# Optimization experiments

Measured on AMD Instinct MI355X. Metric: run time of the kernel, lower is better.

## Reference

```python
import jax, jax.numpy as jnp
import numpy as np

NUM_HEADS = 8

def _heads(x, B, N, H):
    # [B, N, C] -> [B, H, N, d]
    return x.reshape(B, N, H, -1).transpose(0, 2, 1, 3)

def setup_inputs() -> dict:
    key = jax.random.key(0)
    k1, k2, k3, k4 = jax.random.split(key, 4)
    B, N, C = 8, 4096, 512
    x1 = jax.random.normal(k1, (B, N, C), dtype=jnp.float32)
    x2 = jax.random.normal(k2, (B, N, C), dtype=jnp.float32)
    # nn.Linear weights stored as [in, out] for x @ W
    Wkv1 = jax.random.normal(k3, (C, 2 * C), dtype=jnp.float32) * (C ** -0.5)
    Wkv2 = jax.random.normal(k4, (C, 2 * C), dtype=jnp.float32) * (C ** -0.5)
    return {"x1": x1, "x2": x2, "Wkv1": Wkv1, "Wkv2": Wkv2}

def reference(x1, x2, Wkv1, Wkv2):
    B, N, C = x1.shape
    H = NUM_HEADS
    d = C // H
    scale = d ** -0.5

    q1 = _heads(x1, B, N, H)                      # [B,H,N,d]
    q2 = _heads(x2, B, N, H)

    kv1 = (x1 @ Wkv1).reshape(B, N, 2, H, d).transpose(2, 0, 3, 1, 4)
    kv2 = (x2 @ Wkv2).reshape(B, N, 2, H, d).transpose(2, 0, 3, 1, 4)
    k1, v1 = kv1[0], kv1[1]                       # [B,H,N,d]
    k2, v2 = kv2[0], kv2[1]

    # contexts: K^T V over tokens -> small [B,H,d,d]
    ctx1 = jnp.einsum('bhnd,bhne->bhde', k1, v1) * scale
    ctx2 = jnp.einsum('bhnd,bhne->bhde', k2, v2) * scale

    # softmax over dim=-2 (the first d axis), then Q @ ctx
    a1 = jnp.einsum('bhnd,bhde->bhne', q1, jax.nn.softmax(ctx2, axis=-2))
    a2 = jnp.einsum('bhnd,bhde->bhne', q2, jax.nn.softmax(ctx1, axis=-2))

    out1 = a1.transpose(0, 2, 1, 3).reshape(B, N, C)
    out2 = a2.transpose(0, 2, 1, 3).reshape(B, N, C)
    return out1, out2
```

## Files before the change

kernel.cpp:

```cpp
#include <hip/hip_runtime.h>
#include <hip/hip_bf16.h>

typedef __bf16   bf16x8 __attribute__((ext_vector_type(8)));
typedef _Float16 f16x8  __attribute__((ext_vector_type(8)));
typedef _Float16 f16x4  __attribute__((ext_vector_type(4)));
typedef float    f32x4  __attribute__((ext_vector_type(4)));

#define NTOK 4096
#define CDIM 512
#define HEADS 8
#define HD 64

__device__ __forceinline__ void gload_lds16(const void* g, void* l) {
    __builtin_amdgcn_global_load_lds((const __attribute__((address_space(1))) void*)g,
                                     (__attribute__((address_space(3))) void*)l, 16, 0, 0);
}

__global__ __launch_bounds__(256, 3) void xpose_kernel(const float* __restrict__ x1,
                                                       const float* __restrict__ x2,
                                                       const float* __restrict__ Wkv1,
                                                       const float* __restrict__ Wkv2,
                                                       _Float16* __restrict__ xt,
                                                       _Float16* __restrict__ wvt) {
    const int t = threadIdx.x, w = t >> 6, l = t & 63;

    if (blockIdx.x >= 64) {
        if (blockIdx.z >= 8) return;
        const int s = blockIdx.x - 64;
        const float* W = (s ? Wkv2 : Wkv1);
        const int k0 = blockIdx.z * 64;
        const int j = blockIdx.y * 256 + w * 64 + l;

        f16x8 vh[8];
        #pragma unroll
        for (int q = 0; q < 64; ++q) {
            float v = W[(size_t)(k0 + q) * (2 * CDIM) + CDIM + j];
            vh[q >> 3][q & 7] = (_Float16)v;
        }
        _Float16* dh = wvt + ((size_t)s * CDIM + j) * CDIM + k0;
        #pragma unroll
        for (int q = 0; q < 8; ++q)
            *(f16x8*)&dh[q * 8] = vh[q];
        return;
    }

    const int kb = blockIdx.x, cb = blockIdx.y, sb = blockIdx.z;
    const int s = sb >> 3, b = sb & 7;
    const float* xs = (s ? x2 : x1) + (size_t)b * NTOK * CDIM
                    + (size_t)kb * 64 * CDIM + cb * 256;

    __shared__ _Float16 lds[64 * 256];

    float4 v[16];
    #pragma unroll
    for (int i = 0; i < 16; ++i) {
        const int n = 4 * i + w;
        v[i] = *(const float4*)&xs[(size_t)n * CDIM + l * 4];
    }
    #pragma unroll
    for (int i = 0; i < 16; ++i) {
        const int n = 4 * i + w;
        f16x4 p = {(_Float16)v[i].x, (_Float16)v[i].y, (_Float16)v[i].z, (_Float16)v[i].w};
        *(f16x4*)&lds[n * 256 + ((l ^ (n >> 3)) << 2)] = p;
    }
    __syncthreads();

    const int kk8 = (l & 7);
    _Float16* dst = xt + ((size_t)(sb * 64 + kb) * CDIM + cb * 256) * 64;
    #pragma unroll
    for (int q = 0; q < 8; ++q) {
        const int cw = 64 * w + 8 * q + (l >> 3);
        const int c4s = (cw >> 2) ^ kk8, c2 = cw & 3;
        const int base = (c4s << 2) + c2 + kk8 * 8 * 256;
        f16x8 o;
        #pragma unroll
        for (int j = 0; j < 8; ++j)
            o[j] = lds[base + j * 256];
        *(f16x8*)&dst[(size_t)cw * 64 + kk8 * 8] = o;
    }
}

__global__ __launch_bounds__(256) void gram_kernel(const _Float16* __restrict__ xt,
                                                   _Float16* __restrict__ GPh) {
    const int id = blockIdx.x;
    const int vid = (id & 7) * 64 + (id >> 3);
    const int sb = vid >> 5, rest = vid & 31;
    const int split = rest >> 4, tile = rest & 15;
    const int I0 = (tile >> 2) * 128, J0 = (tile & 3) * 128;
    const _Float16* xb = xt + (size_t)sb * CDIM * NTOK;

    __shared__ _Float16 Ih[2][128 * 64];
    __shared__ _Float16 Jh[2][128 * 64];

    const int t = threadIdx.x, w = t >> 6, l = t & 63;
    const int wm = w >> 1, wn = w & 1, l15 = l & 15, lk = l >> 4;
    const int colr = w * 8 + (l >> 3), pos = l & 7;

    f32x4 acc[4][4];
    #pragma unroll
    for (int f = 0; f < 4; ++f)
        #pragma unroll
        for (int g = 0; g < 4; ++g) acc[f][g] = (f32x4)(0.0f);

    auto STAGE = [&](int bufi, int it) {
        const _Float16* kb = xb + (size_t)(split * 32 + it) * CDIM * 64;
        #pragma unroll
        for (int r = 0; r < 4; ++r) {
            const int colw = r * 32 + colr;
            const int swz = ((pos ^ (colw & 7)) << 3);
            gload_lds16(kb + (size_t)(I0 + colw) * 64 + swz, &Ih[bufi][r * 2048 + w * 512]);
            gload_lds16(kb + (size_t)(J0 + colw) * 64 + swz, &Jh[bufi][r * 2048 + w * 512]);
        }
    };

    STAGE(0, 0);
    for (int it = 0; it < 32; ++it) {
        const int cur = it & 1;
        if (it < 31) {
            STAGE(cur ^ 1, it + 1);
            asm volatile("s_waitcnt vmcnt(8)" ::: "memory");
        } else {
            asm volatile("s_waitcnt vmcnt(0)" ::: "memory");
        }
        __builtin_amdgcn_s_barrier();

        const _Float16* Ib = &Ih[cur][0];
        const _Float16* Jb = &Jh[cur][0];
        __builtin_amdgcn_s_setprio(1);
        #pragma unroll
        for (int ks = 0; ks < 2; ++ks) {
            f16x8 a[4], bb[4];
            #pragma unroll
            for (int f = 0; f < 4; ++f) {
                const int i = wm * 64 + f * 16 + l15;
                a[f] = *(const f16x8*)&Ib[i * 64 + ((ks * 4 + lk) ^ (i & 7)) * 8];
            }
            #pragma unroll
            for (int g = 0; g < 4; ++g) {
                const int j = wn * 64 + g * 16 + l15;
                bb[g] = *(const f16x8*)&Jb[j * 64 + ((ks * 4 + lk) ^ (j & 7)) * 8];
            }
            #pragma unroll
            for (int f = 0; f < 4; ++f)
                #pragma unroll
                for (int g = 0; g < 4; ++g)
                    acc[f][g] = __builtin_amdgcn_mfma_f32_16x16x32_f16(a[f], bb[g], acc[f][g], 0, 0, 0);
        }
        __builtin_amdgcn_s_setprio(0);
        __builtin_amdgcn_s_barrier();
    }

    _Float16* Gout = GPh + ((size_t)split * 16 + sb) * CDIM * CDIM;
    #pragma unroll
    for (int f = 0; f < 4; ++f)
        #pragma unroll
        for (int g = 0; g < 4; ++g) {
            const int row0 = I0 + wm * 64 + f * 16 + lk * 4;
            const int col  = J0 + wn * 64 + g * 16 + l15;
            #pragma unroll
            for (int r = 0; r < 4; ++r)
                Gout[(size_t)(row0 + r) * CDIM + col] = (_Float16)acc[f][g][r];
        }
}

__global__ __launch_bounds__(256) void t_kernel(const _Float16* __restrict__ GPh,
                                                const _Float16* __restrict__ wvt,
                                                _Float16* __restrict__ TP) {
    const int id = blockIdx.x;
    const int vid = (id & 7) * 64 + (id >> 3);
    const int sb = vid >> 5, rest = vid & 31;
    const int ks2 = rest >> 4, tile = rest & 15;
    const int s = sb >> 3;
    const int I0 = (tile >> 2) * 128, J0 = (tile & 3) * 128;
    const _Float16* G0 = GPh + (size_t)sb * CDIM * CDIM;
    const _Float16* G1 = GPh + ((size_t)16 + sb) * CDIM * CDIM;
    const _Float16* Bv = wvt + (size_t)s * CDIM * CDIM;

    __shared__ _Float16 Ah[128 * 64];
    __shared__ _Float16 Jh[128 * 64];

    const int t = threadIdx.x, w = t >> 6, l = t & 63;
    const int wm = w >> 1, wn = w & 1, l15 = l & 15, lk = l >> 4;
    const int colr = w * 8 + (l >> 3), pos = l & 7;

    f32x4 acc[4][4];
    #pragma unroll
    for (int f = 0; f < 4; ++f)
        #pragma unroll
        for (int g = 0; g < 4; ++g) acc[f][g] = (f32x4)(0.0f);

    for (int it = 0; it < 4; ++it) {
        const int k0 = ks2 * 256 + it * 64;
        __syncthreads();
        #pragma unroll
        for (int r = 0; r < 4; ++r) {
            const int col = r * 32 + colr;
            const int swz = ((pos ^ (col & 7)) << 3);
            gload_lds16(Bv + (size_t)(J0 + col) * CDIM + k0 + swz, &Jh[r * 2048 + w * 512]);
        }
        #pragma unroll
        for (int r = 0; r < 4; ++r) {
            const int i = r * 32 + (t >> 3), ch = t & 7;
            f16x8 a0 = *(const f16x8*)&G0[(size_t)(I0 + i) * CDIM + k0 + ch * 8];
            f16x8 a1 = *(const f16x8*)&G1[(size_t)(I0 + i) * CDIM + k0 + ch * 8];
            f16x8 sum = a0 + a1;
            *(f16x8*)&Ah[i * 64 + ((ch ^ (i & 7)) << 3)] = sum;
        }
        __syncthreads();
        __builtin_amdgcn_s_setprio(1);
        #pragma unroll
        for (int ks = 0; ks < 2; ++ks) {
            f16x8 a[4], bb[4];
            #pragma unroll
            for (int f = 0; f < 4; ++f) {
                const int i = wm * 64 + f * 16 + l15;
                a[f] = *(const f16x8*)&Ah[i * 64 + ((ks * 4 + lk) ^ (i & 7)) * 8];
            }
            #pragma unroll
            for (int g = 0; g < 4; ++g) {
                const int j = wn * 64 + g * 16 + l15;
                bb[g] = *(const f16x8*)&Jh[j * 64 + ((ks * 4 + lk) ^ (j & 7)) * 8];
            }
            #pragma unroll
            for (int f = 0; f < 4; ++f)
                #pragma unroll
                for (int g = 0; g < 4; ++g)
                    acc[f][g] = __builtin_amdgcn_mfma_f32_16x16x32_f16(a[f], bb[g], acc[f][g], 0, 0, 0);
        }
        __builtin_amdgcn_s_setprio(0);
    }

    _Float16* Tb = TP + ((size_t)ks2 * 16 + sb) * CDIM * CDIM;
    #pragma unroll
    for (int f = 0; f < 4; ++f)
        #pragma unroll
        for (int g = 0; g < 4; ++g) {
            const int row0 = I0 + wm * 64 + f * 16 + lk * 4;
            const int col  = J0 + wn * 64 + g * 16 + l15;
            #pragma unroll
            for (int r = 0; r < 4; ++r)
                Tb[(size_t)(row0 + r) * CDIM + col] = (_Float16)acc[f][g][r];
        }
}

__global__ __launch_bounds__(256) void ctx_gemm_kernel(const _Float16* __restrict__ TP,
                                                       const float* __restrict__ Wkv1,
                                                       const float* __restrict__ Wkv2,
                                                       float* __restrict__ CP) {
    const int h = blockIdx.x, sb = blockIdx.y, kq = blockIdx.z;
    const int s = sb >> 3;
    const float* W  = (s == 0 ? Wkv1 : Wkv2);
    const _Float16* T0 = TP + (size_t)sb * CDIM * CDIM;
    const _Float16* T1 = TP + ((size_t)16 + sb) * CDIM * CDIM;

    __shared__ float Kt[64][65];
    __shared__ float Tt[64][65];

    const int t = threadIdx.x;
    const int td = t >> 4, te = t & 15;
    float acc[4][4] = {};

    for (int it = 0; it < 2; ++it) {
        const int kc = kq * 128 + it * 64;
        __syncthreads();
        for (int i = 0; i < 16; ++i) {
            const int idx = t + i * 256;
            const int r = idx >> 6, cc = idx & 63;
            Kt[r][cc] = W[(size_t)(kc + r) * (2 * CDIM) + h * HD + cc];
            Tt[r][cc] = (float)T0[(size_t)(kc + r) * CDIM + h * HD + cc]
                      + (float)T1[(size_t)(kc + r) * CDIM + h * HD + cc];
        }
        __syncthreads();
        for (int k = 0; k < 64; ++k) {
            float a[4], bb[4];
            #pragma unroll
            for (int i = 0; i < 4; ++i) a[i] = Kt[k][td * 4 + i];
            #pragma unroll
            for (int j = 0; j < 4; ++j) bb[j] = Tt[k][te * 4 + j];
            #pragma unroll
            for (int i = 0; i < 4; ++i)
                #pragma unroll
                for (int j = 0; j < 4; ++j) acc[i][j] += a[i] * bb[j];
        }
    }
    float* out = CP + (size_t)(((kq * 16 + sb) * HEADS) + h) * HD * HD;
    for (int i = 0; i < 4; ++i)
        for (int j = 0; j < 4; ++j)
            out[(size_t)(td * 4 + i) * HD + te * 4 + j] = acc[i][j];
}

__global__ __launch_bounds__(256) void ctx_fin_kernel(const float* __restrict__ CP,
                                                      _Float16* __restrict__ smT) {
    const int h = blockIdx.x, sb = blockIdx.y;

    __shared__ float ctxs[64][65];
    __shared__ float mred[64], sred[64];

    const int t = threadIdx.x;
    const float scale = 0.125f;
    #pragma unroll
    for (int i = 0; i < 4; ++i) {
        const int idx4 = t + i * 256;
        const int d = idx4 >> 4, e4 = idx4 & 15;
        f32x4 sum = (f32x4)(0.0f);
        #pragma unroll
        for (int kq = 0; kq < 4; ++kq) {
            const float* p = CP + (size_t)(((kq * 16 + sb) * HEADS) + h) * HD * HD;
            f32x4 v = *(const f32x4*)&p[d * HD + e4 * 4];
            sum += v;
        }
        *(f32x4*)&ctxs[d][e4 * 4] = sum * scale;
    }
    __syncthreads();
    if (t < 64) {
        float m = -1e30f;
        for (int d = 0; d < 64; ++d) m = fmaxf(m, ctxs[d][t]);
        float ssum = 0.f;
        for (int d = 0; d < 64; ++d) ssum += expf(ctxs[d][t] - m);
        mred[t] = m;
        sred[t] = 1.0f / ssum;
    }
    __syncthreads();
    _Float16* smout = smT + (size_t)(sb * HEADS + h) * HD * HD;
    #pragma unroll
    for (int i = 0; i < 16; ++i) {
        const int idx = t + i * 256;
        const int e = idx >> 6, d = idx & 63;
        smout[e * HD + d] = (_Float16)(expf(ctxs[d][e] - mred[e]) * sred[e]);
    }
}

__global__ __launch_bounds__(256) void out_kernel(const float* __restrict__ x1,
                                                  const float* __restrict__ x2,
                                                  const _Float16* __restrict__ smT,
                                                  float* __restrict__ out) {
    const int id = blockIdx.x;
    const int vid = (id & 7) * 512 + (id >> 3);
    const int h = vid & 7, nt = (vid >> 3) & 31, sb = vid >> 8;
    const int s = sb >> 3, b = sb & 7;
    const float* xs = (s ? x2 : x1) + (size_t)b * NTOK * CDIM;
    const _Float16* sm = smT + (size_t)((((1 - s) * 8 + b) * HEADS) + h) * HD * HD;
    const int n0 = nt * 128;

    __shared__ _Float16 Axt[128 * 64];
    __shared__ _Float16 Bsm[64 * 64];

    const int t = threadIdx.x, w = t >> 6, l = t & 63;
    const int l15 = l & 15, lk = l >> 4;

    #pragma unroll
    for (int r = 0; r < 2; ++r) {
        const int e = r * 32 + w * 8 + (l >> 3), pos = l & 7;
        gload_lds16(sm + (size_t)e * HD + ((pos ^ (e & 7)) << 3), &Bsm[r * 2048 + w * 512]);
    }
    #pragma unroll
    for (int p = 0; p < 8; ++p) {
        const int row = p * 16 + (t >> 4), f4c = t & 15;
        float4 u = *(const float4*)&xs[(size_t)(n0 + row) * CDIM + h * HD + f4c * 4];
        f16x4 q = {(_Float16)u.x, (_Float16)u.y, (_Float16)u.z, (_Float16)u.w};
        const int byte = row * 128 + (((f4c >> 1) ^ (row & 7)) << 4) + ((f4c & 1) << 3);
        *(f16x4*)((char*)Axt + byte) = q;
    }
    __syncthreads();

    f32x4 acc[2][4];
    #pragma unroll
    for (int m = 0; m < 2; ++m)
        #pragma unroll
        for (int g = 0; g < 4; ++g) acc[m][g] = (f32x4)(0.0f);

    #pragma unroll
    for (int ks = 0; ks < 2; ++ks) {
        f16x8 a[2], bb[4];
        #pragma unroll
        for (int m = 0; m < 2; ++m) {
            const int row = w * 32 + m * 16 + l15;
            a[m] = *(const f16x8*)((char*)Axt + row * 128 + (((ks * 4 + lk) ^ (row & 7)) << 4));
        }
        #pragma unroll
        for (int g = 0; g < 4; ++g) {
            const int e = g * 16 + l15;
            bb[g] = *(const f16x8*)((char*)Bsm + e * 128 + (((ks * 4 + lk) ^ (e & 7)) << 4));
        }
        #pragma unroll
        for (int m = 0; m < 2; ++m)
            #pragma unroll
            for (int g = 0; g < 4; ++g)
                acc[m][g] = __builtin_amdgcn_mfma_f32_16x16x32_f16(a[m], bb[g], acc[m][g], 0, 0, 0);
    }

    float* ob = out + (size_t)s * (8ULL * NTOK * CDIM) + (size_t)b * NTOK * CDIM;
    #pragma unroll
    for (int m = 0; m < 2; ++m)
        #pragma unroll
        for (int g = 0; g < 4; ++g) {
            const int row0 = n0 + w * 32 + m * 16 + lk * 4;
            const int col  = h * HD + g * 16 + l15;
            #pragma unroll
            for (int r = 0; r < 4; ++r)
                ob[(size_t)(row0 + r) * CDIM + col] = acc[m][g][r];
        }
}

extern "C" void kernel_launch(void* const* d_in, const int* in_sizes, int n_in,
                              void* d_out, int out_size, void* d_ws, size_t ws_size,
                              hipStream_t stream) {
    const float* x1   = (const float*)d_in[0];
    const float* x2   = (const float*)d_in[1];
    const float* Wkv1 = (const float*)d_in[2];
    const float* Wkv2 = (const float*)d_in[3];
    float* out = (float*)d_out;

    char* base = (char*)d_out;
    _Float16* XT   = (_Float16*)(base + 0);
    _Float16* WVT  = (_Float16*)(base + 67108864);
    _Float16* GPh  = (_Float16*)(base + 68157440);
    _Float16* TP   = (_Float16*)(base + 84934656);
    float*    CP   = (float*)(base + 101711872);
    _Float16* SMT  = (_Float16*)d_ws;

    hipLaunchKernelGGL(xpose_kernel, dim3(66, 2, 16), dim3(256), 0, stream,
                       x1, x2, Wkv1, Wkv2, XT, WVT);
    hipLaunchKernelGGL(gram_kernel, dim3(512), dim3(256), 0, stream, XT, GPh);
    hipLaunchKernelGGL(t_kernel, dim3(512), dim3(256), 0, stream, GPh, WVT, TP);
    hipLaunchKernelGGL(ctx_gemm_kernel, dim3(8, 16, 4), dim3(256), 0, stream,
                       TP, Wkv1, Wkv2, CP);
    hipLaunchKernelGGL(ctx_fin_kernel, dim3(8, 16), dim3(256), 0, stream, CP, SMT);
    hipLaunchKernelGGL(out_kernel, dim3(4096), dim3(256), 0, stream, x1, x2, SMT, out);
}
```

Measured before the change: 152.8 us.

## Split Gram reduction four ways with smaller K tiles for higher occupancy

The Gram kernel now splits the token reduction into four partial sums instead of two, launching twice as many blocks. Each stage loads 32-wide K slices with a new XOR swizzle, which halves LDS use so the kernel can target four blocks per CU. The consumer kernel sums four fp16 partials instead of two, and workspace offsets are moved to hold the extra partials. The aim is better CU fill and latency hiding, at the cost of more partial-sum traffic and an extra fp16 rounding step.

```diff
diff --git a/kernel.cpp b/kernel.cpp
--- a/kernel.cpp
+++ b/kernel.cpp
@@ -80,21 +80,21 @@
     }
 }
 
-__global__ __launch_bounds__(256) void gram_kernel(const _Float16* __restrict__ xt,
-                                                   _Float16* __restrict__ GPh) {
+__global__ __launch_bounds__(256, 4) void gram_kernel(const _Float16* __restrict__ xt,
+                                                      _Float16* __restrict__ GPh) {
     const int id = blockIdx.x;
-    const int vid = (id & 7) * 64 + (id >> 3);
-    const int sb = vid >> 5, rest = vid & 31;
+    const int vid = (id & 7) * 128 + (id >> 3);
+    const int sb = vid >> 6, rest = vid & 63;
     const int split = rest >> 4, tile = rest & 15;
     const int I0 = (tile >> 2) * 128, J0 = (tile & 3) * 128;
     const _Float16* xb = xt + (size_t)sb * CDIM * NTOK;
 
-    __shared__ _Float16 Ih[2][128 * 64];
-    __shared__ _Float16 Jh[2][128 * 64];
+    __shared__ _Float16 Ih[2][128 * 32];
+    __shared__ _Float16 Jh[2][128 * 32];
 
     const int t = threadIdx.x, w = t >> 6, l = t & 63;
     const int wm = w >> 1, wn = w & 1, l15 = l & 15, lk = l >> 4;
-    const int colr = w * 8 + (l >> 3), pos = l & 7;
+    const int scol = w * 16 + (l >> 2), spos = l & 3;
 
     f32x4 acc[4][4];
     #pragma unroll
@@ -103,13 +103,17 @@
         for (int g = 0; g < 4; ++g) acc[f][g] = (f32x4)(0.0f);
 
     auto STAGE = [&](int bufi, int it) {
-        const _Float16* kb = xb + (size_t)(split * 32 + it) * CDIM * 64;
-        #pragma unroll
-        for (int r = 0; r < 4; ++r) {
-            const int colw = r * 32 + colr;
-            const int swz = ((pos ^ (colw & 7)) << 3);
-            gload_lds16(kb + (size_t)(I0 + colw) * 64 + swz, &Ih[bufi][r * 2048 + w * 512]);
-            gload_lds16(kb + (size_t)(J0 + colw) * 64 + swz, &Jh[bufi][r * 2048 + w * 512]);
+        const int kglob = split * 1024 + it * 32;
+        const int kbi = kglob >> 6, khalf = (kglob >> 5) & 1;
+        const _Float16* kbase = xb + (size_t)kbi * (CDIM * 64) + khalf * 32;
+        #pragma unroll
+        for (int r = 0; r < 2; ++r) {
+            const int col = r * 64 + scol;
+            const int kk0 = (spos ^ ((col ^ (col >> 2)) & 3)) * 8;
+            gload_lds16(kbase + (size_t)(I0 + col) * 64 + kk0,
+                        &Ih[bufi][(r * 256 + w * 64) * 8]);
+            gload_lds16(kbase + (size_t)(J0 + col) * 64 + kk0,
+                        &Jh[bufi][(r * 256 + w * 64) * 8]);
         }
     };
 
@@ -118,7 +122,7 @@
         const int cur = it & 1;
         if (it < 31) {
             STAGE(cur ^ 1, it + 1);
-            asm volatile("s_waitcnt vmcnt(8)" ::: "memory");
+            asm volatile("s_waitcnt vmcnt(4)" ::: "memory");
         } else {
             asm volatile("s_waitcnt vmcnt(0)" ::: "memory");
         }
@@ -127,18 +131,17 @@
         const _Float16* Ib = &Ih[cur][0];
         const _Float16* Jb = &Jh[cur][0];
         __builtin_amdgcn_s_setprio(1);
-        #pragma unroll
-        for (int ks = 0; ks < 2; ++ks) {
+        {
             f16x8 a[4], bb[4];
             #pragma unroll
             for (int f = 0; f < 4; ++f) {
                 const int i = wm * 64 + f * 16 + l15;
-                a[f] = *(const f16x8*)&Ib[i * 64 + ((ks * 4 + lk) ^ (i & 7)) * 8];
+                a[f] = *(const f16x8*)&Ib[i * 32 + ((lk ^ ((i ^ (i >> 2)) & 3)) << 3)];
             }
             #pragma unroll
             for (int g = 0; g < 4; ++g) {
                 const int j = wn * 64 + g * 16 + l15;
-                bb[g] = *(const f16x8*)&Jb[j * 64 + ((ks * 4 + lk) ^ (j & 7)) * 8];
+                bb[g] = *(const f16x8*)&Jb[j * 32 + ((lk ^ ((j ^ (j >> 2)) & 3)) << 3)];
             }
             #pragma unroll
             for (int f = 0; f < 4; ++f)
@@ -174,6 +177,8 @@
     const int I0 = (tile >> 2) * 128, J0 = (tile & 3) * 128;
     const _Float16* G0 = GPh + (size_t)sb * CDIM * CDIM;
     const _Float16* G1 = GPh + ((size_t)16 + sb) * CDIM * CDIM;
+    const _Float16* G2 = GPh + ((size_t)32 + sb) * CDIM * CDIM;
+    const _Float16* G3 = GPh + ((size_t)48 + sb) * CDIM * CDIM;
     const _Float16* Bv = wvt + (size_t)s * CDIM * CDIM;
 
     __shared__ _Float16 Ah[128 * 64];
@@ -201,9 +206,12 @@
         #pragma unroll
         for (int r = 0; r < 4; ++r) {
             const int i = r * 32 + (t >> 3), ch = t & 7;
-            f16x8 a0 = *(const f16x8*)&G0[(size_t)(I0 + i) * CDIM + k0 + ch * 8];
-            f16x8 a1 = *(const f16x8*)&G1[(size_t)(I0 + i) * CDIM + k0 + ch * 8];
-            f16x8 sum = a0 + a1;
+            const size_t off = (size_t)(I0 + i) * CDIM + k0 + ch * 8;
+            f16x8 a0 = *(const f16x8*)&G0[off];
+            f16x8 a1 = *(const f16x8*)&G1[off];
+            f16x8 a2 = *(const f16x8*)&G2[off];
+            f16x8 a3 = *(const f16x8*)&G3[off];
+            f16x8 sum = (a0 + a1) + (a2 + a3);
             *(f16x8*)&Ah[i * 64 + ((ch ^ (i & 7)) << 3)] = sum;
         }
         __syncthreads();
@@ -415,13 +423,13 @@
     _Float16* XT   = (_Float16*)(base + 0);
     _Float16* WVT  = (_Float16*)(base + 67108864);
     _Float16* GPh  = (_Float16*)(base + 68157440);
-    _Float16* TP   = (_Float16*)(base + 84934656);
-    float*    CP   = (float*)(base + 101711872);
+    _Float16* TP   = (_Float16*)(base + 101711872);
+    float*    CP   = (float*)(base + 118489088);
     _Float16* SMT  = (_Float16*)d_ws;
 
     hipLaunchKernelGGL(xpose_kernel, dim3(66, 2, 16), dim3(256), 0, stream,
                        x1, x2, Wkv1, Wkv2, XT, WVT);
-    hipLaunchKernelGGL(gram_kernel, dim3(512), dim3(256), 0, stream, XT, GPh);
+    hipLaunchKernelGGL(gram_kernel, dim3(1024), dim3(256), 0, stream, XT, GPh);
     hipLaunchKernelGGL(t_kernel, dim3(512), dim3(256), 0, stream, GPh, WVT, TP);
     hipLaunchKernelGGL(ctx_gemm_kernel, dim3(8, 16, 4), dim3(256), 0, stream,
                        TP, Wkv1, Wkv2, CP);
```

Measured after the change: 159.8 us. 4.6% more time.
